# Kernel optimization log

Hardware: AMD Instinct MI355X
Metric: run time of the kernel (lower is better)

Reference implementation:

```python
import jax, jax.numpy as jnp
import numpy as np


def setup_inputs() -> dict:
    key = jax.random.key(0)
    k1, k2, k3, k4 = jax.random.split(key, 4)
    B, N, F_in, F_out = 8, 2048, 256, 128
    h = jax.random.normal(k1, (B, N, F_in), dtype=jnp.float32)
    # fc: Linear(in_features, out_features, bias=False); store as [F_in, F_out]
    W_fc = jax.random.normal(k2, (F_in, F_out), dtype=jnp.float32) * (1.0 / np.sqrt(F_in))
    # attn_fc: Linear(2*F_out, 1, bias=False) -> split into the two additive halves
    a_i = jax.random.normal(k3, (F_out,), dtype=jnp.float32) * (1.0 / np.sqrt(2 * F_out))
    a_j = jax.random.normal(k4, (F_out,), dtype=jnp.float32) * (1.0 / np.sqrt(2 * F_out))
    return {"h": h, "W_fc": W_fc, "a_i": a_i, "a_j": a_j}


def reference(h, W_fc, a_i, a_j):
    # Wh: [B, N, F_out]
    Wh = jnp.einsum("bnf,fo->bno", h, W_fc)
    # attn_fc(cat([Wh_i, Wh_j])) is linear, so it decomposes additively:
    # e[b,i,j] = <Wh[b,i], a_i> + <Wh[b,j], a_j>  -- same math, no N^2*2F tensor
    s_i = Wh @ a_i  # [B, N]
    s_j = Wh @ a_j  # [B, N]
    e = s_i[:, :, None] + s_j[:, None, :]  # [B, N, N]
    alpha = jax.nn.softmax(jax.nn.leaky_relu(e, negative_slope=0.01), axis=-1)
    h_prime = jnp.einsum("bij,bjo->bio", alpha, Wh)  # [B, N, F_out]
    return h_prime
```

## Files before the change

kernel.cpp:

```cpp
#include <hip/hip_runtime.h>
#include <hip/hip_bf16.h>

#define BATCH 8
#define NN 2048
#define FIN 256
#define FOUT 128
#define ROWS (BATCH*NN)
#define NP1 (NN+1)
#define SEGS 128
#define SLEN (NN/SEGS)

typedef __attribute__((ext_vector_type(8))) __bf16 bf16x8;
typedef __attribute__((ext_vector_type(4))) float f32x4;
typedef __attribute__((ext_vector_type(8))) unsigned short ushort8_t;

__device__ __forceinline__ unsigned pack2(float a, float b){
  __hip_bfloat16 x = __float2bfloat16(a), y = __float2bfloat16(b);
  unsigned short ux = *(unsigned short*)&x, uy = *(unsigned short*)&y;
  return ((unsigned)uy << 16) | (unsigned)ux;
}
__device__ __forceinline__ float lo2f(unsigned u){ union{unsigned v;float f;}c; c.v = u << 16; return c.f; }
__device__ __forceinline__ float hi2f(unsigned u){ union{unsigned v;float f;}c; c.v = u & 0xffff0000u; return c.f; }

__device__ __forceinline__ void bsplit(float x, unsigned short& hu, unsigned short& lu){
  __hip_bfloat16 hb = __float2bfloat16(x);
  hu = *(unsigned short*)&hb;
  union{unsigned u; float f;} hf; hf.u = (unsigned)hu << 16;
  __hip_bfloat16 lb = __float2bfloat16(x - hf.f);
  lu = *(unsigned short*)&lb;
}

__global__ __launch_bounds__(256) void k_wsplit(const float* __restrict__ W,
                                                unsigned short* __restrict__ Wth,
                                                unsigned short* __restrict__ Wtl){
  const int gid = blockIdx.x * 256 + threadIdx.x;
  const int k = gid >> 5, c4 = (gid & 31) * 4;
  float4 v = *(const float4*)&W[(size_t)k * FOUT + c4];
  float xs[4] = {v.x, v.y, v.z, v.w};
  #pragma unroll
  for (int i = 0; i < 4; i++){
    unsigned short hu, lu;
    bsplit(xs[i], hu, lu);
    Wth[(size_t)(c4 + i) * FIN + k] = hu;
    Wtl[(size_t)(c4 + i) * FIN + k] = lu;
  }
}

__global__ __launch_bounds__(256) void k_gemm(const float* __restrict__ h,
                                              const unsigned short* __restrict__ Wth,
                                              const unsigned short* __restrict__ Wtl,
                                              const float* __restrict__ ai,
                                              const float* __restrict__ aj,
                                              float* __restrict__ Wh,
                                              float* __restrict__ sI,
                                              float* __restrict__ sJ){
  __shared__ unsigned short Ah[32*40], Al[32*40];
  __shared__ unsigned short Bh[128*40], Bl[128*40];
  __shared__ float spI[2][32], spJ[2][32];
  const int t = threadIdx.x;
  const int rbase = blockIdx.x * 32;
  const int w = t >> 6, l = t & 63;
  const int g = w & 1, cg = w >> 1;
  const int lr = l & 15, lq = l >> 4;
  const int sar = t >> 3, sak = (t & 7) * 4;
  const int sbc = t >> 1, sbh = (t & 1) * 16;

  f32x4 acc[4];
  #pragma unroll
  for (int ct = 0; ct < 4; ct++) acc[ct] = (f32x4){0.f, 0.f, 0.f, 0.f};

  for (int k0 = 0; k0 < FIN; k0 += 32){
    {
      float4 hv = *(const float4*)&h[(size_t)(rbase + sar) * FIN + k0 + sak];
      float xs[4] = {hv.x, hv.y, hv.z, hv.w};
      ushort4 hh, ll;
      unsigned short hu, lu;
      bsplit(xs[0], hu, lu); hh.x = hu; ll.x = lu;
      bsplit(xs[1], hu, lu); hh.y = hu; ll.y = lu;
      bsplit(xs[2], hu, lu); hh.z = hu; ll.z = lu;
      bsplit(xs[3], hu, lu); hh.w = hu; ll.w = lu;
      *(ushort4*)&Ah[sar * 40 + sak] = hh;
      *(ushort4*)&Al[sar * 40 + sak] = ll;
    }
    {
      const size_t gb = (size_t)sbc * FIN + k0 + sbh;
      ushort8_t b0 = *(const ushort8_t*)&Wth[gb];
      ushort8_t b1 = *(const ushort8_t*)&Wth[gb + 8];
      ushort8_t c0 = *(const ushort8_t*)&Wtl[gb];
      ushort8_t c1 = *(const ushort8_t*)&Wtl[gb + 8];
      *(ushort8_t*)&Bh[sbc * 40 + sbh]     = b0;
      *(ushort8_t*)&Bh[sbc * 40 + sbh + 8] = b1;
      *(ushort8_t*)&Bl[sbc * 40 + sbh]     = c0;
      *(ushort8_t*)&Bl[sbc * 40 + sbh + 8] = c1;
    }
    __syncthreads();
    const bf16x8 avh = __builtin_bit_cast(bf16x8, *(const ushort8_t*)&Ah[(g*16 + lr)*40 + lq*8]);
    const bf16x8 avl = __builtin_bit_cast(bf16x8, *(const ushort8_t*)&Al[(g*16 + lr)*40 + lq*8]);
    #pragma unroll
    for (int ct = 0; ct < 4; ct++){
      const int col = cg*64 + ct*16 + lr;
      const bf16x8 bvh = __builtin_bit_cast(bf16x8, *(const ushort8_t*)&Bh[col*40 + lq*8]);
      const bf16x8 bvl = __builtin_bit_cast(bf16x8, *(const ushort8_t*)&Bl[col*40 + lq*8]);
      acc[ct] = __builtin_amdgcn_mfma_f32_16x16x32_bf16(avh, bvh, acc[ct], 0, 0, 0);
      acc[ct] = __builtin_amdgcn_mfma_f32_16x16x32_bf16(avh, bvl, acc[ct], 0, 0, 0);
      acc[ct] = __builtin_amdgcn_mfma_f32_16x16x32_bf16(avl, bvh, acc[ct], 0, 0, 0);
    }
    __syncthreads();
  }
  float pi[4] = {0.f,0.f,0.f,0.f}, pj[4] = {0.f,0.f,0.f,0.f};
  #pragma unroll
  for (int ct = 0; ct < 4; ct++){
    const int col = cg*64 + ct*16 + lr;
    const float fai = ai[col], faj = aj[col];
    #pragma unroll
    for (int q = 0; q < 4; q++){
      const float val = acc[ct][q];
      Wh[(size_t)(rbase + g*16 + lq*4 + q) * FOUT + col] = val;
      pi[q] = fmaf(val, fai, pi[q]);
      pj[q] = fmaf(val, faj, pj[q]);
    }
  }
  #pragma unroll
  for (int q = 0; q < 4; q++){
    #pragma unroll
    for (int m = 1; m < 16; m <<= 1){
      pi[q] += __shfl_xor(pi[q], m);
      pj[q] += __shfl_xor(pj[q], m);
    }
  }
  if (lr == 0){
    #pragma unroll
    for (int q = 0; q < 4; q++){
      spI[cg][g*16 + lq*4 + q] = pi[q];
      spJ[cg][g*16 + lq*4 + q] = pj[q];
    }
  }
  __syncthreads();
  if (t < 32){
    sI[rbase + t] = spI[0][t] + spI[1][t];
    sJ[rbase + t] = spJ[0][t] + spJ[1][t];
  }
}

__global__ __launch_bounds__(256) void k_rank_scatter(const float* __restrict__ sJ,
                                                      float* __restrict__ sortedS,
                                                      int* __restrict__ perm,
                                                      float2* __restrict__ e12g){
  const int b = blockIdx.x >> 6;
  const int jc = blockIdx.x & 63;
  __shared__ float v[NN];
  __shared__ int partial[8][32];
  const int t = threadIdx.x;
  const float* sj = sJ + b * NN;
  #pragma unroll
  for (int u = 0; u < 2; u++)
    ((float4*)v)[t + u * 256] = ((const float4*)sj)[t + u * 256];
  const int jj = t & 31, qq = t >> 5;
  const int j = jc * 32 + jj;
  const float x = sj[j];
  __syncthreads();
  const int q0 = qq * 256;
  int r = 0;
  #pragma unroll 8
  for (int q4 = 0; q4 < 64; q4++){
    const int q = q0 + q4 * 4;
    float4 y = *(const float4*)&v[q];
    r += (y.x < x) || (y.x == x && (q + 0) < j);
    r += (y.y < x) || (y.y == x && (q + 1) < j);
    r += (y.z < x) || (y.z == x && (q + 2) < j);
    r += (y.w < x) || (y.w == x && (q + 3) < j);
  }
  partial[qq][jj] = r;
  __syncthreads();
  if (t < 32){
    int R = 0;
    #pragma unroll
    for (int q8 = 0; q8 < 8; q8++) R += partial[q8][t];
    const int myj = jc * 32 + t;
    const float xx = v[myj];
    sortedS[b * NN + R] = xx;
    perm[b * NN + R] = myj;
    e12g[b * NN + R] = make_float2(expf(xx), expf(0.01f * xx));
  }
}

__global__ __launch_bounds__(512) void k_fuse(const float2* __restrict__ e12g,
                                              const float* __restrict__ Wh,
                                              const int* __restrict__ perm,
                                              float2* __restrict__ abPre,
                                              unsigned* __restrict__ P12){
  const int t = threadIdx.x;
  if (blockIdx.x < BATCH){
    const int b = blockIdx.x;
    __shared__ float p1[512], p2[512];
    const float2* e12 = e12g + b * NN;
    float l1[4], l2[4];
    float s1 = 0.f, s2 = 0.f;
    #pragma unroll
    for (int q = 0; q < 4; q++){
      float2 v = e12[t * 4 + q];
      s1 += v.x; l1[q] = s1;
      s2 += v.y; l2[q] = s2;
    }
    p1[t] = s1; p2[t] = s2;
    __syncthreads();
    #pragma unroll
    for (int d = 1; d < 512; d <<= 1){
      const float u1 = (t >= d) ? p1[t - d] : 0.f;
      const float u2 = (t >= d) ? p2[t - d] : 0.f;
      __syncthreads();
      if (t >= d){ p1[t] += u1; p2[t] += u2; }
      __syncthreads();
    }
    const float b1 = p1[t] - s1, b2 = p2[t] - s2;
    float2* abP = abPre + b * NP1;
    #pragma unroll
    for (int q = 0; q < 4; q++)
      abP[1 + t * 4 + q] = make_float2(b1 + l1[q], b2 + l2[q]);
    if (t == 0) abP[0] = make_float2(0.f, 0.f);
    return;
  }
  const int bc = blockIdx.x - BATCH;
  const int b = bc >> 5;
  const int og = bc & 31;
  const int ol = t & 3;
  const int o = og * 4 + ol;
  const int seg = t >> 2;
  const int r0 = seg * SLEN;
  __shared__ float p1[SEGS][4], p2[SEGS][4];
  const int*    pm  = perm + b * NN;
  const float2* e12 = e12g + b * NN;
  const float* whb = Wh + (size_t)b * NN * FOUT;
  float w[SLEN];
  float t1 = 0.f, t2 = 0.f;
  #pragma unroll
  for (int r = 0; r < SLEN; r++){
    w[r] = whb[(size_t)pm[r0 + r] * FOUT + o];
    const float2 u = e12[r0 + r];
    t1 = fmaf(u.x, w[r], t1);
    t2 = fmaf(u.y, w[r], t2);
  }
  p1[seg][ol] = t1; p2[seg][ol] = t2;
  __syncthreads();
  #pragma unroll
  for (int d = 1; d < SEGS; d <<= 1){
    const float u1 = (seg >= d) ? p1[seg - d][ol] : 0.f;
    const float u2 = (seg >= d) ? p2[seg - d][ol] : 0.f;
    __syncthreads();
    if (seg >= d){ p1[seg][ol] += u1; p2[seg][ol] += u2; }
    __syncthreads();
  }
  float acc1 = p1[seg][ol] - t1;
  float acc2 = p2[seg][ol] - t2;
  unsigned* pp = P12 + ((size_t)(b * 32 + og) * NP1) * 4 + ol;
  if (seg == 0) pp[0] = 0u;
  #pragma unroll
  for (int r = 0; r < SLEN; r++){
    const float2 u = e12[r0 + r];
    acc1 = fmaf(u.x, w[r], acc1);
    acc2 = fmaf(u.y, w[r], acc2);
    pp[(size_t)(r0 + r + 1) * 4] = pack2(acc1, acc2);
  }
}

__global__ __launch_bounds__(256) void k_out(const float* __restrict__ sI,
                                             const float* __restrict__ sortedS,
                                             const float2* __restrict__ abPre,
                                             const unsigned* __restrict__ P12,
                                             float* __restrict__ out){
  const int row = blockIdx.x * 2 + (threadIdx.x >> 7);
  const int b = row >> 11;
  const float s = sI[row];
  const float key = -s;
  const float* ss = sortedS + b * NN;
  int lo = 0, hi = NN;
  while (lo < hi){
    int mid = (lo + hi) >> 1;
    if (ss[mid] <= key) lo = mid + 1; else hi = mid;
  }
  const int k = lo;
  const float w1 = expf(s), w2 = expf(0.01f * s);
  const float2* abP = abPre + b * NP1;
  const float2 vT = abP[NN];
  const float2 vk = abP[k];
  const float inv = 1.0f / (w1 * (vT.x - vk.x) + w2 * vk.y);
  const int o = threadIdx.x & 127;
  const size_t pbase = (size_t)(b * 32 + (o >> 2)) * NP1;
  const unsigned uk = P12[(pbase + k)  * 4 + (o & 3)];
  const unsigned uT = P12[(pbase + NN) * 4 + (o & 3)];
  float num = w1 * (lo2f(uT) - lo2f(uk)) + w2 * hi2f(uk);
  out[(size_t)row * FOUT + o] = num * inv;
}

extern "C" void kernel_launch(void* const* d_in, const int* in_sizes, int n_in,
                              void* d_out, int out_size, void* d_ws, size_t ws_size,
                              hipStream_t stream){
  const float* h  = (const float*)d_in[0];
  const float* W  = (const float*)d_in[1];
  const float* ai = (const float*)d_in[2];
  const float* aj = (const float*)d_in[3];
  float* out = (float*)d_out;

  char* ws = (char*)d_ws;
  size_t off = 0;
  auto alloc = [&](size_t bytes) -> void* {
    void* p = ws + off;
    off += (bytes + 255) & ~(size_t)255;
    return p;
  };
  float*          Wh   = (float*)   alloc((size_t)ROWS * FOUT * 4);
  float*          sI   = (float*)   alloc((size_t)ROWS * 4);
  float*          sJ   = (float*)   alloc((size_t)ROWS * 4);
  float*          sortedS = (float*)alloc((size_t)BATCH * NN * 4);
  int*            perm = (int*)     alloc((size_t)BATCH * NN * 4);
  float2*         e12  = (float2*)  alloc((size_t)BATCH * NN * 8);
  float2*         abPre= (float2*)  alloc((size_t)BATCH * NP1 * 8);
  unsigned*       P12  = (unsigned*)alloc((size_t)BATCH * 32 * NP1 * 4 * 4);
  unsigned short* Wth  = (unsigned short*)alloc((size_t)FOUT * FIN * 2);
  unsigned short* Wtl  = (unsigned short*)alloc((size_t)FOUT * FIN * 2);

  k_wsplit      <<<32, 256, 0, stream>>>(W, Wth, Wtl);
  k_gemm        <<<ROWS / 32, 256, 0, stream>>>(h, Wth, Wtl, ai, aj, Wh, sI, sJ);
  k_rank_scatter<<<BATCH * 64, 256, 0, stream>>>(sJ, sortedS, perm, e12);
  k_fuse        <<<BATCH + BATCH * 32, 512, 0, stream>>>(e12, Wh, perm, abPre, P12);
  k_out         <<<ROWS / 2, 256, 0, stream>>>(sI, sortedS, abPre, P12, out);
}
```

Baseline: 126.5 us.

## Fuse prefix-sum and output kernels, keeping prefix tables in shared memory

Merges k_fuse and k_out into one kernel. Each block builds its per-output-column prefix tables (P12 and the scalar abPre prefix) in LDS instead of writing them to global memory. It then runs a batched 16-way binary search over an LDS copy of sortedS and writes the outputs directly. This removes one launch and the global round trip of the large P12 table. The cost is 256 blocks with heavy LDS use (about 58KB) and redundant scalar prefix and search work in every block, which may limit occupancy and parallelism.

Result: faster. 116.3 us (-8.1%).

```diff
diff --git a/kernel.cpp b/kernel.cpp
--- a/kernel.cpp
+++ b/kernel.cpp
@@ -184,112 +184,116 @@
   }
 }
 
-__global__ __launch_bounds__(512) void k_fuse(const float2* __restrict__ e12g,
-                                              const float* __restrict__ Wh,
-                                              const int* __restrict__ perm,
-                                              float2* __restrict__ abPre,
-                                              unsigned* __restrict__ P12){
-  const int t = threadIdx.x;
-  if (blockIdx.x < BATCH){
-    const int b = blockIdx.x;
-    __shared__ float p1[512], p2[512];
-    const float2* e12 = e12g + b * NN;
-    float l1[4], l2[4];
-    float s1 = 0.f, s2 = 0.f;
-    #pragma unroll
-    for (int q = 0; q < 4; q++){
-      float2 v = e12[t * 4 + q];
-      s1 += v.x; l1[q] = s1;
-      s2 += v.y; l2[q] = s2;
-    }
-    p1[t] = s1; p2[t] = s2;
-    __syncthreads();
-    #pragma unroll
-    for (int d = 1; d < 512; d <<= 1){
-      const float u1 = (t >= d) ? p1[t - d] : 0.f;
-      const float u2 = (t >= d) ? p2[t - d] : 0.f;
-      __syncthreads();
-      if (t >= d){ p1[t] += u1; p2[t] += u2; }
-      __syncthreads();
-    }
-    const float b1 = p1[t] - s1, b2 = p2[t] - s2;
-    float2* abP = abPre + b * NP1;
-    #pragma unroll
-    for (int q = 0; q < 4; q++)
-      abP[1 + t * 4 + q] = make_float2(b1 + l1[q], b2 + l2[q]);
-    if (t == 0) abP[0] = make_float2(0.f, 0.f);
-    return;
-  }
-  const int bc = blockIdx.x - BATCH;
+__global__ __launch_bounds__(512) void k_fuseout(const float* __restrict__ sortedS,
+                                                 const float* __restrict__ sI,
+                                                 const float2* __restrict__ e12g,
+                                                 const float* __restrict__ Wh,
+                                                 const int* __restrict__ perm,
+                                                 float* __restrict__ out){
+  __shared__ float    ssL[NN];
+  __shared__ float2   abL[NP1];
+  __shared__ unsigned PL[NP1][4];
+  __shared__ float p1[SEGS][4], p2[SEGS][4];
+  __shared__ float p1s[SEGS], p2s[SEGS];
+  const int bc = blockIdx.x;
   const int b = bc >> 5;
   const int og = bc & 31;
+  const int t = threadIdx.x;
   const int ol = t & 3;
   const int o = og * 4 + ol;
   const int seg = t >> 2;
   const int r0 = seg * SLEN;
-  __shared__ float p1[SEGS][4], p2[SEGS][4];
+
+  const float* ssg = sortedS + b * NN;
+  #pragma unroll
+  for (int u = 0; u < 4; u++) ssL[t + u * 512] = ssg[t + u * 512];
+
   const int*    pm  = perm + b * NN;
   const float2* e12 = e12g + b * NN;
-  const float* whb = Wh + (size_t)b * NN * FOUT;
-  float w[SLEN];
-  float t1 = 0.f, t2 = 0.f;
+  const float*  whb = Wh + (size_t)b * NN * FOUT;
+  float w[SLEN], ex[SLEN], ey[SLEN];
+  float t1 = 0.f, t2 = 0.f, s1 = 0.f, s2 = 0.f;
   #pragma unroll
   for (int r = 0; r < SLEN; r++){
     w[r] = whb[(size_t)pm[r0 + r] * FOUT + o];
     const float2 u = e12[r0 + r];
+    ex[r] = u.x; ey[r] = u.y;
     t1 = fmaf(u.x, w[r], t1);
     t2 = fmaf(u.y, w[r], t2);
+    s1 += u.x; s2 += u.y;
   }
   p1[seg][ol] = t1; p2[seg][ol] = t2;
+  if (ol == 0){ p1s[seg] = s1; p2s[seg] = s2; }
   __syncthreads();
   #pragma unroll
   for (int d = 1; d < SEGS; d <<= 1){
     const float u1 = (seg >= d) ? p1[seg - d][ol] : 0.f;
     const float u2 = (seg >= d) ? p2[seg - d][ol] : 0.f;
+    const float v1 = (ol == 0 && seg >= d) ? p1s[seg - d] : 0.f;
+    const float v2 = (ol == 0 && seg >= d) ? p2s[seg - d] : 0.f;
     __syncthreads();
-    if (seg >= d){ p1[seg][ol] += u1; p2[seg][ol] += u2; }
+    if (seg >= d){
+      p1[seg][ol] += u1; p2[seg][ol] += u2;
+      if (ol == 0){ p1s[seg] += v1; p2s[seg] += v2; }
+    }
     __syncthreads();
   }
   float acc1 = p1[seg][ol] - t1;
   float acc2 = p2[seg][ol] - t2;
-  unsigned* pp = P12 + ((size_t)(b * 32 + og) * NP1) * 4 + ol;
-  if (seg == 0) pp[0] = 0u;
-  #pragma unroll
-  for (int r = 0; r < SLEN; r++){
-    const float2 u = e12[r0 + r];
-    acc1 = fmaf(u.x, w[r], acc1);
-    acc2 = fmaf(u.y, w[r], acc2);
-    pp[(size_t)(r0 + r + 1) * 4] = pack2(acc1, acc2);
-  }
-}
-
-__global__ __launch_bounds__(256) void k_out(const float* __restrict__ sI,
-                                             const float* __restrict__ sortedS,
-                                             const float2* __restrict__ abPre,
-                                             const unsigned* __restrict__ P12,
-                                             float* __restrict__ out){
-  const int row = blockIdx.x * 2 + (threadIdx.x >> 7);
-  const int b = row >> 11;
-  const float s = sI[row];
-  const float key = -s;
-  const float* ss = sortedS + b * NN;
-  int lo = 0, hi = NN;
-  while (lo < hi){
-    int mid = (lo + hi) >> 1;
-    if (ss[mid] <= key) lo = mid + 1; else hi = mid;
-  }
-  const int k = lo;
-  const float w1 = expf(s), w2 = expf(0.01f * s);
-  const float2* abP = abPre + b * NP1;
-  const float2 vT = abP[NN];
-  const float2 vk = abP[k];
-  const float inv = 1.0f / (w1 * (vT.x - vk.x) + w2 * vk.y);
-  const int o = threadIdx.x & 127;
-  const size_t pbase = (size_t)(b * 32 + (o >> 2)) * NP1;
-  const unsigned uk = P12[(pbase + k)  * 4 + (o & 3)];
-  const unsigned uT = P12[(pbase + NN) * 4 + (o & 3)];
-  float num = w1 * (lo2f(uT) - lo2f(uk)) + w2 * hi2f(uk);
-  out[(size_t)row * FOUT + o] = num * inv;
+  if (seg == 0){
+    PL[0][ol] = 0u;
+    if (ol == 0) abL[0] = make_float2(0.f, 0.f);
+  }
+  {
+    float offs1 = 0.f, offs2 = 0.f;
+    if (ol == 0){ offs1 = p1s[seg] - s1; offs2 = p2s[seg] - s2; }
+    float run1 = 0.f, run2 = 0.f;
+    #pragma unroll
+    for (int r = 0; r < SLEN; r++){
+      acc1 = fmaf(ex[r], w[r], acc1);
+      acc2 = fmaf(ey[r], w[r], acc2);
+      PL[r0 + r + 1][ol] = pack2(acc1, acc2);
+      if (ol == 0){
+        run1 += ex[r]; run2 += ey[r];
+        abL[r0 + r + 1] = make_float2(offs1 + run1, offs2 + run2);
+      }
+    }
+  }
+  __syncthreads();
+  const int tg = t >> 2;
+  float sv[16];
+  #pragma unroll
+  for (int u = 0; u < 16; u++) sv[u] = sI[b * NN + tg + u * 128];
+  int lo[16], hi[16];
+  #pragma unroll
+  for (int u = 0; u < 16; u++){ lo[u] = 0; hi[u] = NN; }
+  #pragma unroll
+  for (int step = 0; step < 11; step++){
+    float mv[16]; int mid[16];
+    #pragma unroll
+    for (int u = 0; u < 16; u++){
+      mid[u] = (lo[u] + hi[u]) >> 1;
+      mv[u] = ssL[mid[u]];
+    }
+    #pragma unroll
+    for (int u = 0; u < 16; u++){
+      if (mv[u] <= -sv[u]) lo[u] = mid[u] + 1; else hi[u] = mid[u];
+    }
+  }
+  const float2 vT = abL[NN];
+  const unsigned uTp = PL[NN][ol];
+  #pragma unroll
+  for (int u = 0; u < 16; u++){
+    const int row = tg + u * 128;
+    const int k = lo[u];
+    const float s = sv[u];
+    const float w1 = expf(s), w2 = expf(0.01f * s);
+    const float2 vk = abL[k];
+    const float inv = 1.0f / (w1 * (vT.x - vk.x) + w2 * vk.y);
+    const unsigned uk = PL[k][ol];
+    const float num = w1 * (lo2f(uTp) - lo2f(uk)) + w2 * hi2f(uk);
+    out[(size_t)(b * NN + row) * FOUT + o] = num * inv;
+  }
 }
 
 extern "C" void kernel_launch(void* const* d_in, const int* in_sizes, int n_in,
@@ -314,14 +318,11 @@
   float*          sortedS = (float*)alloc((size_t)BATCH * NN * 4);
   int*            perm = (int*)     alloc((size_t)BATCH * NN * 4);
   float2*         e12  = (float2*)  alloc((size_t)BATCH * NN * 8);
-  float2*         abPre= (float2*)  alloc((size_t)BATCH * NP1 * 8);
-  unsigned*       P12  = (unsigned*)alloc((size_t)BATCH * 32 * NP1 * 4 * 4);
   unsigned short* Wth  = (unsigned short*)alloc((size_t)FOUT * FIN * 2);
   unsigned short* Wtl  = (unsigned short*)alloc((size_t)FOUT * FIN * 2);
 
   k_wsplit      <<<32, 256, 0, stream>>>(W, Wth, Wtl);
   k_gemm        <<<ROWS / 32, 256, 0, stream>>>(h, Wth, Wtl, ai, aj, Wh, sI, sJ);
   k_rank_scatter<<<BATCH * 64, 256, 0, stream>>>(sJ, sortedS, perm, e12);
-  k_fuse        <<<BATCH + BATCH * 32, 512, 0, stream>>>(e12, Wh, perm, abPre, P12);
-  k_out         <<<ROWS / 2, 256, 0, stream>>>(sI, sortedS, abPre, P12, out);
-}
+  k_fuseout     <<<BATCH * 32, 512, 0, stream>>>(sortedS, sI, e12, Wh, perm, out);
+}
```
